# Kernel tuning notes

Measured on AMD Instinct MI355X. Metric: run time of the kernel, lower is better.

Reference implementation:

```python
import jax, jax.numpy as jnp
import numpy as np

LEVELS = [(128, 128), (64, 64), (32, 32), (16, 16)]  # (h, w) per level
NUM_HEADS = 8
NUM_LEVELS = 4
NUM_POINTS = 4
EMBED_DIMS = 256


def _bilinear_sample(img, gx, gy):
    """grid_sample(mode='bilinear', padding_mode='zeros', align_corners=False).
    img: (B, H, W, C); gx, gy: (B, N) in [-1, 1]. Returns (B, N, C)."""
    B, H, W, C = img.shape
    x = ((gx + 1.0) * W - 1.0) * 0.5
    y = ((gy + 1.0) * H - 1.0) * 0.5
    x0 = jnp.floor(x)
    y0 = jnp.floor(y)
    wx1 = x - x0
    wy1 = y - y0
    flat = img.reshape(B, H * W, C)

    def gather(xf, yf, w):
        xi = xf.astype(jnp.int32)
        yi = yf.astype(jnp.int32)
        valid = (xi >= 0) & (xi < W) & (yi >= 0) & (yi < H)
        idx = jnp.clip(yi, 0, H - 1) * W + jnp.clip(xi, 0, W - 1)
        v = jnp.take_along_axis(flat, idx[..., None], axis=1)
        return v * (w * valid)[..., None]

    return (gather(x0, y0, (1 - wx1) * (1 - wy1))
            + gather(x0 + 1, y0, wx1 * (1 - wy1))
            + gather(x0, y0 + 1, (1 - wx1) * wy1)
            + gather(x0 + 1, y0 + 1, wx1 * wy1))


def _msda(value, sampling_locations, attention_weights):
    """value: (bs, nv, nh, dh); sampling_locations: (bs, nq, nh, L, P, 2);
    attention_weights: (bs, nq, nh, L, P). Returns (bs, nq, nh*dh)."""
    bs, nv, nh, dh = value.shape
    nq = sampling_locations.shape[1]
    P = sampling_locations.shape[4]
    grids = 2.0 * sampling_locations - 1.0
    out = jnp.zeros((bs * nh, nq, dh), value.dtype)
    start = 0
    for l, (h, w) in enumerate(LEVELS):
        v = value[:, start:start + h * w]                      # (bs, h*w, nh, dh)
        start += h * w
        v = v.transpose(0, 2, 1, 3).reshape(bs * nh, h, w, dh)
        g = grids[:, :, :, l].transpose(0, 2, 1, 3, 4).reshape(bs * nh, nq * P, 2)
        s = _bilinear_sample(v, g[..., 0], g[..., 1]).reshape(bs * nh, nq, P, dh)
        wgt = attention_weights[:, :, :, l].transpose(0, 2, 1, 3).reshape(bs * nh, nq, P)
        out = out + jnp.einsum('bqpd,bqp->bqd', s, wgt)
    return out.reshape(bs, nh, nq, dh).transpose(0, 2, 1, 3).reshape(bs, nq, nh * dh)


def setup_inputs() -> dict:
    key = jax.random.key(0)
    ks = jax.random.split(key, 12)
    bs, nq, D = 2, sum(h * w for h, w in LEVELS), EMBED_DIMS
    spatial_shapes = jnp.array(LEVELS, dtype=jnp.int32)
    starts = np.cumsum([0] + [h * w for h, w in LEVELS[:-1]])
    return {
        'query': jax.random.normal(ks[0], (bs, nq, D), jnp.float32),
        'value': jax.random.normal(ks[1], (bs, nq, D), jnp.float32),
        'reference_points': jax.random.uniform(ks[2], (bs, nq, NUM_LEVELS, 2), jnp.float32),
        'spatial_shapes': spatial_shapes,
        'level_start_index': jnp.asarray(starts, dtype=jnp.int32),
        'Wv': jax.random.normal(ks[3], (D, D), jnp.float32) * 0.02,
        'bv': jnp.zeros((D,), jnp.float32),
        'Wo': jax.random.normal(ks[4], (D, NUM_HEADS * NUM_LEVELS * NUM_POINTS * 2), jnp.float32) * 0.02,
        'bo': jax.random.normal(ks[5], (NUM_HEADS * NUM_LEVELS * NUM_POINTS * 2,), jnp.float32) * 0.5,
        'Wa': jax.random.normal(ks[6], (D, NUM_HEADS * NUM_LEVELS * NUM_POINTS), jnp.float32) * 0.02,
        'ba': jnp.zeros((NUM_HEADS * NUM_LEVELS * NUM_POINTS,), jnp.float32),
        'Wout': jax.random.normal(ks[7], (D, D), jnp.float32) * 0.02,
        'bout': jnp.zeros((D,), jnp.float32),
    }


def reference(query, value, reference_points, spatial_shapes, level_start_index,
              Wv, bv, Wo, bo, Wa, ba, Wout, bout):
    bs, nq, D = query.shape
    nv = value.shape[1]
    nh, L, P = NUM_HEADS, NUM_LEVELS, NUM_POINTS
    dh = D // nh
    identity = query

    v = (value @ Wv + bv).reshape(bs, nv, nh, dh)
    offs = (query @ Wo + bo).reshape(bs, nq, nh, L, P, 2)
    attw = jax.nn.softmax((query @ Wa + ba).reshape(bs, nq, nh, L * P), axis=-1)
    attw = attw.reshape(bs, nq, nh, L, P)

    # offset_normalizer = (w, h) per level
    norm = jnp.stack([spatial_shapes[:, 1], spatial_shapes[:, 0]], -1).astype(query.dtype)
    sampling_locations = (reference_points[:, :, None, :, None, :]
                          + offs / norm[None, None, None, :, None, :])

    out = _msda(v, sampling_locations, attw)
    out = out @ Wout + bout
    return out + identity  # dropout is identity in eval
```

## Files before the change

kernel.cpp:

```cpp
#include <hip/hip_runtime.h>
#include <hip/hip_fp16.h>

#define BS 2
#define NQ 21760
#define NV 21760
#define DIM 256
#define NH 8
#define DH 32
#define NL 4
#define NP 4

typedef __attribute__((ext_vector_type(8))) _Float16 f16x8;
typedef __attribute__((ext_vector_type(4))) float f32x4;

__device__ __forceinline__ unsigned short f2h(float f) {
    return __half_as_ushort(__float2half(f));
}
__device__ __forceinline__ float h2f(unsigned short s) {
    return __half2float(__ushort_as_half(s));
}

__global__ __launch_bounds__(64) void k_wprep(
    const float* __restrict__ Wo, const float* __restrict__ Wa,
    const float* __restrict__ Wv, const float* __restrict__ Wout,
    unsigned short* __restrict__ wsw)
{
    const int tile = blockIdx.x;
    const int lane = threadIdx.x;
    const float* W; int N, nb, kb;
    if (tile < 192) { nb = tile >> 3; kb = tile & 7;
        if (nb < 16) { W = Wo; N = 256; } else { W = Wa; N = 128; nb -= 16; } }
    else if (tile < 320) { int tt = tile - 192; nb = tt >> 3; kb = tt & 7; W = Wv;   N = 256; }
    else               { int tt = tile - 320; nb = tt >> 3; kb = tt & 7; W = Wout; N = 256; }
    const int quad = lane >> 4, l15 = lane & 15;
    const int col = nb * 16 + l15;
    unsigned int pk[4];
#pragma unroll
    for (int jj = 0; jj < 4; jj++) {
        int k0 = kb * 32 + quad * 8 + jj * 2;
        pk[jj] = (unsigned int)f2h(W[(size_t)k0 * N + col])
               | ((unsigned int)f2h(W[(size_t)(k0 + 1) * N + col]) << 16);
    }
    *(uint4*)(wsw + (size_t)tile * 512 + lane * 8) = *(const uint4*)pk;
}

__device__ __forceinline__ void stage32_f32(const float* __restrict__ src,
                                            unsigned short* __restrict__ As)
{
    const int t = threadIdx.x;
    const int colg = t & 63;
    const int row0 = t >> 6;
#pragma unroll
    for (int i = 0; i < 8; i++) {
        int row = row0 + i * 4;
        float4 f = ((const float4*)(src + (size_t)row * 256))[colg];
        uint2 p;
        p.x = (unsigned int)f2h(f.x) | ((unsigned int)f2h(f.y) << 16);
        p.y = (unsigned int)f2h(f.z) | ((unsigned int)f2h(f.w) << 16);
        *(uint2*)&As[row * 264 + colg * 4] = p;
    }
}
__device__ __forceinline__ void stage32_h16(const unsigned short* __restrict__ src,
                                            unsigned short* __restrict__ As)
{
    const int t = threadIdx.x;
    const int colg = t & 63;
    const int row0 = t >> 6;
#pragma unroll
    for (int i = 0; i < 8; i++) {
        int row = row0 + i * 4;
        uint2 u = ((const uint2*)(src + (size_t)row * 256))[colg];
        *(uint2*)&As[row * 264 + colg * 4] = u;
    }
}

template<int M>
__device__ __forceinline__ void gemm32(const unsigned short* __restrict__ As,
                                       const unsigned short* __restrict__ wswb,
                                       int mt0, f32x4 acc[][2], int lane)
{
    const int quad = lane >> 4, l15 = lane & 15;
#pragma unroll
    for (int kh = 0; kh < 2; kh++) {
        f16x8 aw[M][4];
#pragma unroll
        for (int m = 0; m < M; m++)
#pragma unroll
            for (int j = 0; j < 4; j++)
                aw[m][j] = *(const f16x8*)(wswb +
                    ((((mt0 + m) * 8 + kh * 4 + j) << 9) + (lane << 3)));
#pragma unroll
        for (int j = 0; j < 4; j++) {
            const int kb = kh * 4 + j;
            f16x8 dq[2];
#pragma unroll
            for (int n = 0; n < 2; n++)
                dq[n] = *(const f16x8*)&As[(n * 16 + l15) * 264 + kb * 32 + quad * 8];
#pragma unroll
            for (int m = 0; m < M; m++)
#pragma unroll
                for (int n = 0; n < 2; n++)
                    acc[m][n] = __builtin_amdgcn_mfma_f32_16x16x32_f16(aw[m][j], dq[n], acc[m][n], 0, 0, 0);
        }
    }
}

__global__ __launch_bounds__(256) void k_proj(
    const float* __restrict__ value,
    const float* __restrict__ query,
    const float* __restrict__ refp,
    const unsigned short* __restrict__ wsw,
    const float* __restrict__ bv,
    const float* __restrict__ bo,
    const float* __restrict__ ba,
    unsigned short* __restrict__ v_hm,
    float* __restrict__ locs_ws,
    unsigned short* __restrict__ attw_b)
{
    __shared__ unsigned short As[32 * 264];
    const int t = threadIdx.x;
    const int w = t >> 6, lane = t & 63;
    const int quad = lane >> 4, l15 = lane & 15;

    if (blockIdx.x < 1360) {
        const int tile = blockIdx.x;
        const int r0i = tile * 32;
        const int bb = (tile >= 680);
        const int pix0 = r0i - bb * NV;
        stage32_f32(value + (size_t)r0i * 256, As);
        __syncthreads();
        f32x4 acc[4][2];
#pragma unroll
        for (int m = 0; m < 4; m++)
#pragma unroll
            for (int n = 0; n < 2; n++) acc[m][n] = (f32x4){0.f, 0.f, 0.f, 0.f};
        gemm32<4>(As, wsw + 98304, w * 4, acc, lane);
#pragma unroll
        for (int m = 0; m < 4; m++) {
            const int col = w * 64 + m * 16 + quad * 4;
            const int h = col >> 5, ch = col & 31;
            const float4 bias = *(const float4*)(bv + col);
            unsigned short* __restrict__ vh =
                v_hm + ((size_t)(bb * NH + h) * NV + pix0) * DH + ch;
#pragma unroll
            for (int n = 0; n < 2; n++) {
                f32x4 a = acc[m][n];
                uint2 o;
                o.x = (unsigned int)f2h(a[0] + bias.x)
                    | ((unsigned int)f2h(a[1] + bias.y) << 16);
                o.y = (unsigned int)f2h(a[2] + bias.z)
                    | ((unsigned int)f2h(a[3] + bias.w) << 16);
                *(uint2*)(vh + (size_t)(n * 16 + l15) * DH) = o;
            }
        }
    } else {
        const int qb = blockIdx.x - 1360;
        const int rt = qb >> 1, ch2 = qb & 1;
        const size_t r0 = (size_t)rt * 32;
        stage32_f32(query + r0 * 256, As);
        __syncthreads();
        f32x4 acc[3][2];
#pragma unroll
        for (int m = 0; m < 3; m++)
#pragma unroll
            for (int n = 0; n < 2; n++) acc[m][n] = (f32x4){0.f, 0.f, 0.f, 0.f};
        const int mt0 = ch2 * 12 + w * 3;
        gemm32<3>(As, wsw, mt0, acc, lane);
#pragma unroll
        for (int m = 0; m < 3; m++) {
            const int mt = mt0 + m;
            if (mt < 16) {
                const int c0 = mt * 16 + quad * 4;
                const int l = (c0 >> 3) & 3;
                const float rnorm = 1.f / (float)(128 >> l);
                const float4 bias = *(const float4*)(bo + c0);
#pragma unroll
                for (int n = 0; n < 2; n++) {
                    size_t row = r0 + n * 16 + l15;
                    float2 ref = *(const float2*)(refp + row * 8 + l * 2);
                    f32x4 a = acc[m][n];
                    float4 o;
                    o.x = ref.x + (a[0] + bias.x) * rnorm;
                    o.y = ref.y + (a[1] + bias.y) * rnorm;
                    o.z = ref.x + (a[2] + bias.z) * rnorm;
                    o.w = ref.y + (a[3] + bias.w) * rnorm;
                    *(float4*)(locs_ws + row * 256 + c0) = o;
                }
            } else {
                const int c0 = (mt - 16) * 16 + quad * 4;
                const float4 bias = *(const float4*)(ba + c0);
#pragma unroll
                for (int n = 0; n < 2; n++) {
                    size_t row = r0 + n * 16 + l15;
                    f32x4 a = acc[m][n];
                    float v0 = a[0] + bias.x, v1 = a[1] + bias.y;
                    float v2 = a[2] + bias.z, v3 = a[3] + bias.w;
                    float mm = fmaxf(fmaxf(v0, v1), fmaxf(v2, v3));
                    mm = fmaxf(mm, __shfl_xor(mm, 16, 64));
                    mm = fmaxf(mm, __shfl_xor(mm, 32, 64));
                    float e0 = __expf(v0 - mm), e1 = __expf(v1 - mm);
                    float e2 = __expf(v2 - mm), e3 = __expf(v3 - mm);
                    float s = (e0 + e1) + (e2 + e3);
                    s += __shfl_xor(s, 16, 64);
                    s += __shfl_xor(s, 32, 64);
                    float rs = 1.f / s;
                    uint2 o;
                    o.x = (unsigned int)f2h(e0 * rs) | ((unsigned int)f2h(e1 * rs) << 16);
                    o.y = (unsigned int)f2h(e2 * rs) | ((unsigned int)f2h(e3 * rs) << 16);
                    *(uint2*)(attw_b + row * 128 + c0) = o;
                }
            }
        }
    }
}

__device__ __forceinline__ void acc4(float wf, uint2 d,
                                     float& a0, float& a1, float& a2, float& a3)
{
    __half2 lo = *(__half2*)&d.x;
    __half2 hi = *(__half2*)&d.y;
    a0 = fmaf(wf, __half2float(__low2half(lo)),  a0);
    a1 = fmaf(wf, __half2float(__high2half(lo)), a1);
    a2 = fmaf(wf, __half2float(__low2half(hi)),  a2);
    a3 = fmaf(wf, __half2float(__high2half(hi)), a3);
}

__global__ __launch_bounds__(256) void k_sample(
    const unsigned short* __restrict__ v_hm,
    const float* __restrict__ locs_ws,
    const unsigned short* __restrict__ attw_b,
    unsigned short* __restrict__ msda_ws)
{
    __shared__ uint2 tap[16 * 4 * 32];
    const int t = threadIdx.x;
    const int bid = blockIdx.x;

    const int xcd  = bid & 7;
    const int slot = bid >> 3;
    const int sub  = (slot >= 680) ? 1 : 0;
    const int chunk = slot - sub * 680;
    const int pair = xcd * 2 + sub;
    const int b = pair & 1;
    const int h = pair >> 1;
    const int q0 = chunk * 32;

#pragma unroll
    for (int i = 0; i < 2; i++) {
        const int tapid = t + i * 256;
        const int q  = tapid & 31;
        const int tp = tapid >> 5;
        const size_t row = (size_t)(b * NQ + q0 + q);
        float2 xy = *(const float2*)(locs_ws + row * 256 + h * 32 + tp * 2);
        float a   = h2f(attw_b[row * 128 + h * 16 + tp]);

        const int l = tp >> 2;
        const int Wl = 128 >> l;
        const float Wf = (float)Wl;
        const int start = (l == 0) ? 0 : (l == 1) ? 16384 : (l == 2) ? 20480 : 21504;
        float x = xy.x * Wf - 0.5f;
        float y = xy.y * Wf - 0.5f;
        float xf = floorf(x), yf = floorf(y);
        int x0 = (int)xf, y0 = (int)yf;
        float wx1 = x - xf, wy1 = y - yf;
        float wx0 = 1.f - wx1, wy0 = 1.f - wy1;
#pragma unroll
        for (int c = 0; c < 4; c++) {
            const int dx = c & 1, dy = c >> 1;
            int xi = x0 + dx, yi = y0 + dy;
            bool valid = (xi >= 0) & (xi < Wl) & (yi >= 0) & (yi < Wl);
            int xc = min(max(xi, 0), Wl - 1);
            int yc = min(max(yi, 0), Wl - 1);
            float wc = valid ? a * (dx ? wx1 : wx0) * (dy ? wy1 : wy0) : 0.f;
            uint2 rec;
            rec.x = __float_as_uint(wc);
            rec.y = ((unsigned int)(start + yc * Wl + xc)) * 64u;
            tap[(tp * 4 + c) * 32 + q] = rec;
        }
    }
    __syncthreads();

    const int w4   = t >> 6;
    const int lane = t & 63;
    const int ql   = lane >> 3;
    const int c4   = lane & 7;
    const int q    = w4 * 8 + ql;
    const unsigned int c4off = (unsigned int)c4 * 8u;
    const char* __restrict__ vb =
        (const char*)(v_hm + (size_t)(b * NH + h) * NV * DH);

    float a0 = 0.f, a1 = 0.f, a2 = 0.f, a3 = 0.f;
#pragma unroll
    for (int ti = 0; ti < 16; ti++) {
        uint2 r0 = tap[(ti * 4 + 0) * 32 + q];
        uint2 r1 = tap[(ti * 4 + 1) * 32 + q];
        uint2 r2 = tap[(ti * 4 + 2) * 32 + q];
        uint2 r3 = tap[(ti * 4 + 3) * 32 + q];
        uint2 d0 = *(const uint2*)(vb + (r0.y + c4off));
        uint2 d1 = *(const uint2*)(vb + (r1.y + c4off));
        uint2 d2 = *(const uint2*)(vb + (r2.y + c4off));
        uint2 d3 = *(const uint2*)(vb + (r3.y + c4off));
        acc4(__uint_as_float(r0.x), d0, a0, a1, a2, a3);
        acc4(__uint_as_float(r1.x), d1, a0, a1, a2, a3);
        acc4(__uint_as_float(r2.x), d2, a0, a1, a2, a3);
        acc4(__uint_as_float(r3.x), d3, a0, a1, a2, a3);
    }
    uint2 o;
    o.x = (unsigned int)f2h(a0) | ((unsigned int)f2h(a1) << 16);
    o.y = (unsigned int)f2h(a2) | ((unsigned int)f2h(a3) << 16);
    *(uint2*)(msda_ws + (size_t)(b * NQ + q0 + q) * DIM + h * DH + c4 * 4) = o;
}

__global__ __launch_bounds__(256) void k_out_mfma(
    const unsigned short* __restrict__ msda_ws,
    const unsigned short* __restrict__ wswo,
    const float* __restrict__ bout,
    const float* __restrict__ query,
    float* __restrict__ out)
{
    __shared__ unsigned short As[32 * 264];
    const int t = threadIdx.x;
    const int w = t >> 6, lane = t & 63;
    const int quad = lane >> 4, l15 = lane & 15;
    const size_t r0 = (size_t)blockIdx.x * 32;

    stage32_h16(msda_ws + r0 * 256, As);
    __syncthreads();

    f32x4 acc[4][2];
#pragma unroll
    for (int m = 0; m < 4; m++)
#pragma unroll
        for (int n = 0; n < 2; n++) acc[m][n] = (f32x4){0.f, 0.f, 0.f, 0.f};
    gemm32<4>(As, wswo, w * 4, acc, lane);

#pragma unroll
    for (int m = 0; m < 4; m++) {
        const int c0 = w * 64 + m * 16 + quad * 4;
        const float4 bias = *(const float4*)(bout + c0);
#pragma unroll
        for (int n = 0; n < 2; n++) {
            size_t row = r0 + n * 16 + l15;
            float4 q4 = *(const float4*)(query + row * 256 + c0);
            f32x4 a = acc[m][n];
            float4 o;
            o.x = a[0] + bias.x + q4.x;
            o.y = a[1] + bias.y + q4.y;
            o.z = a[2] + bias.z + q4.z;
            o.w = a[3] + bias.w + q4.w;
            *(float4*)(out + row * 256 + c0) = o;
        }
    }
}

extern "C" void kernel_launch(void* const* d_in, const int* in_sizes, int n_in,
                              void* d_out, int out_size, void* d_ws, size_t ws_size,
                              hipStream_t stream)
{
    const float* query = (const float*)d_in[0];
    const float* value = (const float*)d_in[1];
    const float* refp  = (const float*)d_in[2];
    const float* Wv   = (const float*)d_in[5];
    const float* bv   = (const float*)d_in[6];
    const float* Wo   = (const float*)d_in[7];
    const float* bo   = (const float*)d_in[8];
    const float* Wa   = (const float*)d_in[9];
    const float* ba   = (const float*)d_in[10];
    const float* Wout = (const float*)d_in[11];
    const float* bout = (const float*)d_in[12];
    float* out = (float*)d_out;

    char* ws = (char*)d_ws;
    unsigned short* v_hm = (unsigned short*)ws;    ws += (size_t)BS * NH * NV * DH * 2;
    float* locs_ws = (float*)ws;                   ws += (size_t)BS * NQ * DIM * 4;
    unsigned short* attw_b = (unsigned short*)ws;  ws += (size_t)BS * NQ * 128 * 2;
    unsigned short* msda_ws = (unsigned short*)ws; ws += (size_t)BS * NQ * DIM * 2;
    unsigned short* wsw = (unsigned short*)ws;

    k_wprep   <<<448, 64,  0, stream>>>(Wo, Wa, Wv, Wout, wsw);
    k_proj    <<<4080, 256, 0, stream>>>(value, query, refp, wsw, bv, bo, ba,
                                         v_hm, locs_ws, attw_b);
    k_sample  <<<10880, 256, 0, stream>>>(v_hm, locs_ws, attw_b, msda_ws);
    k_out_mfma<<<1360, 256, 0, stream>>>(msda_ws, wsw + 163840, bout, query, out);
}
```

Before: 307.4 us.

## Gather horizontal bilinear tap pairs with 16-byte loads in sampling kernel

The sampling kernel now merges each pair of horizontally adjacent bilinear corners into a single record. That record points at a clamped base column, and each 8-lane group loads 128 contiguous bytes (two pixels × 32 fp16 channels) with 16-byte loads. Lanes 0-3 apply the left-corner weight and lanes 4-7 the right-corner weight, and the two halves are combined with a shuffle before a 16-byte store. This halves the number of gather load instructions and LDS record reads per query, and pads the LDS record array to avoid bank conflicts. In exchange, half the lanes do no useful store, and edge clamping needs extra weight-selection logic.

```diff
diff --git a/kernel.cpp b/kernel.cpp
--- a/kernel.cpp
+++ b/kernel.cpp
@@ -214,15 +214,20 @@
     }
 }
 
-__device__ __forceinline__ void acc4(float wf, uint2 d,
-                                     float& a0, float& a1, float& a2, float& a3)
-{
-    __half2 lo = *(__half2*)&d.x;
-    __half2 hi = *(__half2*)&d.y;
-    a0 = fmaf(wf, __half2float(__low2half(lo)),  a0);
-    a1 = fmaf(wf, __half2float(__high2half(lo)), a1);
-    a2 = fmaf(wf, __half2float(__low2half(hi)),  a2);
-    a3 = fmaf(wf, __half2float(__high2half(hi)), a3);
+__device__ __forceinline__ void acc8(float wf, uint4 d, float* ac)
+{
+    __half2 p0 = *(__half2*)&d.x;
+    __half2 p1 = *(__half2*)&d.y;
+    __half2 p2 = *(__half2*)&d.z;
+    __half2 p3 = *(__half2*)&d.w;
+    ac[0] = fmaf(wf, __half2float(__low2half(p0)),  ac[0]);
+    ac[1] = fmaf(wf, __half2float(__high2half(p0)), ac[1]);
+    ac[2] = fmaf(wf, __half2float(__low2half(p1)),  ac[2]);
+    ac[3] = fmaf(wf, __half2float(__high2half(p1)), ac[3]);
+    ac[4] = fmaf(wf, __half2float(__low2half(p2)),  ac[4]);
+    ac[5] = fmaf(wf, __half2float(__high2half(p2)), ac[5]);
+    ac[6] = fmaf(wf, __half2float(__low2half(p3)),  ac[6]);
+    ac[7] = fmaf(wf, __half2float(__high2half(p3)), ac[7]);
 }
 
 __global__ __launch_bounds__(256) void k_sample(
@@ -231,7 +236,7 @@
     const unsigned short* __restrict__ attw_b,
     unsigned short* __restrict__ msda_ws)
 {
-    __shared__ uint2 tap[16 * 4 * 32];
+    __shared__ uint4 tap[16 * 2 * 33];
     const int t = threadIdx.x;
     const int bid = blockIdx.x;
 
@@ -246,9 +251,9 @@
 
 #pragma unroll
     for (int i = 0; i < 2; i++) {
-        const int tapid = t + i * 256;
-        const int q  = tapid & 31;
-        const int tp = tapid >> 5;
+        const int item = t + i * 256;
+        const int tp = item & 15;
+        const int q  = item >> 4;
         const size_t row = (size_t)(b * NQ + q0 + q);
         float2 xy = *(const float2*)(locs_ws + row * 256 + h * 32 + tp * 2);
         float a   = h2f(attw_b[row * 128 + h * 16 + tp]);
@@ -261,20 +266,24 @@
         float y = xy.y * Wf - 0.5f;
         float xf = floorf(x), yf = floorf(y);
         int x0 = (int)xf, y0 = (int)yf;
-        float wx1 = x - xf, wy1 = y - yf;
-        float wx0 = 1.f - wx1, wy0 = 1.f - wy1;
-#pragma unroll
-        for (int c = 0; c < 4; c++) {
-            const int dx = c & 1, dy = c >> 1;
-            int xi = x0 + dx, yi = y0 + dy;
-            bool valid = (xi >= 0) & (xi < Wl) & (yi >= 0) & (yi < Wl);
-            int xc = min(max(xi, 0), Wl - 1);
+        float wx1 = x - xf, wx0 = 1.f - wx1;
+        float wy1 = y - yf, wy0 = 1.f - wy1;
+        const int base = min(max(x0, 0), Wl - 2);
+        const int sh = x0 - base;
+        const float wxA = (sh == 0) ? wx0 : (sh == -1) ? wx1 : 0.f;
+        const float wxB = (sh == 0) ? wx1 : (sh == 1)  ? wx0 : 0.f;
+#pragma unroll
+        for (int dy = 0; dy < 2; dy++) {
+            int yi = y0 + dy;
+            bool yv = (yi >= 0) && (yi < Wl);
             int yc = min(max(yi, 0), Wl - 1);
-            float wc = valid ? a * (dx ? wx1 : wx0) * (dy ? wy1 : wy0) : 0.f;
-            uint2 rec;
-            rec.x = __float_as_uint(wc);
-            rec.y = ((unsigned int)(start + yc * Wl + xc)) * 64u;
-            tap[(tp * 4 + c) * 32 + q] = rec;
+            float wY = yv ? a * (dy ? wy1 : wy0) : 0.f;
+            uint4 rec;
+            rec.x = __float_as_uint(wY * wxA);
+            rec.y = __float_as_uint(wY * wxB);
+            rec.z = (unsigned int)(start + yc * Wl + base) * 64u;
+            rec.w = 0u;
+            tap[(tp * 2 + dy) * 33 + q] = rec;
         }
     }
     __syncthreads();
@@ -282,32 +291,31 @@
     const int w4   = t >> 6;
     const int lane = t & 63;
     const int ql   = lane >> 3;
-    const int c4   = lane & 7;
+    const int g    = lane & 7;
     const int q    = w4 * 8 + ql;
-    const unsigned int c4off = (unsigned int)c4 * 8u;
+    const bool selA = (g < 4);
+    const unsigned int goff = (unsigned int)g * 16u;
     const char* __restrict__ vb =
         (const char*)(v_hm + (size_t)(b * NH + h) * NV * DH);
 
-    float a0 = 0.f, a1 = 0.f, a2 = 0.f, a3 = 0.f;
-#pragma unroll
-    for (int ti = 0; ti < 16; ti++) {
-        uint2 r0 = tap[(ti * 4 + 0) * 32 + q];
-        uint2 r1 = tap[(ti * 4 + 1) * 32 + q];
-        uint2 r2 = tap[(ti * 4 + 2) * 32 + q];
-        uint2 r3 = tap[(ti * 4 + 3) * 32 + q];
-        uint2 d0 = *(const uint2*)(vb + (r0.y + c4off));
-        uint2 d1 = *(const uint2*)(vb + (r1.y + c4off));
-        uint2 d2 = *(const uint2*)(vb + (r2.y + c4off));
-        uint2 d3 = *(const uint2*)(vb + (r3.y + c4off));
-        acc4(__uint_as_float(r0.x), d0, a0, a1, a2, a3);
-        acc4(__uint_as_float(r1.x), d1, a0, a1, a2, a3);
-        acc4(__uint_as_float(r2.x), d2, a0, a1, a2, a3);
-        acc4(__uint_as_float(r3.x), d3, a0, a1, a2, a3);
-    }
-    uint2 o;
-    o.x = (unsigned int)f2h(a0) | ((unsigned int)f2h(a1) << 16);
-    o.y = (unsigned int)f2h(a2) | ((unsigned int)f2h(a3) << 16);
-    *(uint2*)(msda_ws + (size_t)(b * NQ + q0 + q) * DIM + h * DH + c4 * 4) = o;
+    float ac[8] = {0.f, 0.f, 0.f, 0.f, 0.f, 0.f, 0.f, 0.f};
+#pragma unroll
+    for (int it = 0; it < 32; it++) {
+        uint4 rec = tap[it * 33 + q];
+        float wf = __uint_as_float(selA ? rec.x : rec.y);
+        uint4 d = *(const uint4*)(vb + (rec.z + goff));
+        acc8(wf, d, ac);
+    }
+#pragma unroll
+    for (int k = 0; k < 8; k++) ac[k] += __shfl_xor(ac[k], 4, 64);
+    if (selA) {
+        uint4 o;
+        o.x = (unsigned int)f2h(ac[0]) | ((unsigned int)f2h(ac[1]) << 16);
+        o.y = (unsigned int)f2h(ac[2]) | ((unsigned int)f2h(ac[3]) << 16);
+        o.z = (unsigned int)f2h(ac[4]) | ((unsigned int)f2h(ac[5]) << 16);
+        o.w = (unsigned int)f2h(ac[6]) | ((unsigned int)f2h(ac[7]) << 16);
+        *(uint4*)(msda_ws + (size_t)(b * NQ + q0 + q) * DIM + h * DH + g * 8) = o;
+    }
 }
 
 __global__ __launch_bounds__(256) void k_out_mfma(
```

Result: faster. 266.0 us (-13.5%).
